# Kernel tuning notes

Hardware: AMD Instinct MI355X
Metric: run time of the kernel (lower is better)

## Reference

```python
import jax, jax.numpy as jnp
import numpy as np

DIM = 512
HEADS = 8
DIM_HEAD = 64
SCALE = DIM_HEAD ** -0.5


def setup_inputs() -> dict:
    key = jax.random.key(0)
    k1, k2, k3, k4, k5 = jax.random.split(key, 5)
    inner = HEADS * DIM_HEAD
    x = jax.random.normal(k1, (16, DIM, 32, 32), dtype=jnp.float32)
    W_proj = jax.random.normal(k2, (DIM, inner * 3), dtype=jnp.float32) * (DIM ** -0.5)
    b_proj = jax.random.normal(k3, (inner * 3,), dtype=jnp.float32) * 0.01
    W_out = jax.random.normal(k4, (inner, DIM), dtype=jnp.float32) * (inner ** -0.5)
    b_out = jax.random.normal(k5, (DIM,), dtype=jnp.float32) * 0.01
    return {"x": x, "W_proj": W_proj, "b_proj": b_proj, "W_out": W_out, "b_out": b_out}


def reference(x, W_proj, b_proj, W_out, b_out):
    b, c, hh, ww = x.shape
    s = hh * ww
    xs = x.reshape(b, c, s).transpose(0, 2, 1)  # b s c
    qkv = xs @ W_proj + b_proj                  # b s (heads * 3*dim_head)
    qkv = qkv.reshape(b, s, HEADS, 3 * DIM_HEAD)
    q, k, v = jnp.split(qkv, 3, axis=-1)        # each: b s h d
    w = jnp.einsum('bshd,bthd->bsth', q, k) * SCALE
    w = jax.nn.softmax(w, axis=2)
    res = jnp.einsum('bsth,bthd->bshd', w, v).reshape(b, s, HEADS * DIM_HEAD)
    out = res @ W_out + b_out + xs              # b s c (residual)
    return out.transpose(0, 2, 1).reshape(b, c, hh, ww)
```

## Files before the change

kernel.cpp:

```cpp
#include <hip/hip_runtime.h>
#include <hip/hip_bf16.h>

#define BATCH 16
#define CDIM  512
#define SEQ   1024
#define HEADS 8
#define DHEAD 64
#define N3    1536
#define QSCALE 0.18033688011112042f

typedef unsigned short ushort_t;
typedef __attribute__((ext_vector_type(8))) short short8;
typedef __attribute__((ext_vector_type(4))) float f32x4;

__device__ __forceinline__ unsigned f2bf(float f) {
    unsigned u = __float_as_uint(f);
    u += 0x7fffu + ((u >> 16) & 1u);
    return u >> 16;
}
__device__ __forceinline__ float fast_exp2(float x) {
    float r;
    asm("v_exp_f32 %0, %1" : "=v"(r) : "v"(x));
    return r;
}
__device__ __forceinline__ unsigned pack_bf16_trunc(float lo, float hi) {
    return __builtin_amdgcn_perm(__float_as_uint(hi), __float_as_uint(lo), 0x07060302u);
}
__device__ __forceinline__ void async16(const void* g, void* l) {
    __builtin_amdgcn_global_load_lds(
        (const __attribute__((address_space(1))) unsigned int*)g,
        (__attribute__((address_space(3))) unsigned int*)l, 16, 0, 0);
}


__global__ __launch_bounds__(256) void blockify_kernel(
    const float* __restrict__ in, ushort_t* __restrict__ out, int C)
{
    __shared__ float t[64][65];
    const int k0 = blockIdx.y * 64, c0 = blockIdx.x * 64;
    const float* inb = in + (size_t)blockIdx.z * 512 * C;
    const int tid = threadIdx.x;
#pragma unroll
    for (int i = 0; i < 16; ++i) {
        int idx = tid + i * 256;
        int r = idx >> 6, c = idx & 63;
        t[r][c] = inb[(size_t)(k0 + r) * C + c0 + c];
    }
    __syncthreads();
    const size_t mbase = (size_t)blockIdx.z * C + c0;
    const int ml = tid & 63;
#pragma unroll
    for (int i = 0; i < 2; ++i) {
        int oct = (tid >> 6) + i * 4;
        size_t m = mbase + ml;
        int mt = (int)(m >> 7), mr = (int)(m & 127);
        int m16 = mr >> 4, col = mr & 15;
        int k = k0 + oct * 8;
        int it = k >> 5, q = (k >> 3) & 3;
        uint4 pk;
        pk.x = f2bf(t[oct * 8 + 0][ml]) | (f2bf(t[oct * 8 + 1][ml]) << 16);
        pk.y = f2bf(t[oct * 8 + 2][ml]) | (f2bf(t[oct * 8 + 3][ml]) << 16);
        pk.z = f2bf(t[oct * 8 + 4][ml]) | (f2bf(t[oct * 8 + 5][ml]) << 16);
        pk.w = f2bf(t[oct * 8 + 6][ml]) | (f2bf(t[oct * 8 + 7][ml]) << 16);
        size_t off = ((size_t)(mt * 16 + it) * 8 + m16) * 512 + (q * 16 + col) * 8;
        *(uint4*)&out[off] = pk;
    }
}

__global__ __launch_bounds__(256) void qkv_gemm_kernel(
    const ushort_t* __restrict__ xtb, const ushort_t* __restrict__ WpTb,
    const float* __restrict__ bp,
    ushort_t* __restrict__ q_buf, ushort_t* __restrict__ kb,
    ushort_t* __restrict__ vb)
{
    __shared__ alignas(16) ushort_t Asub[2][8 * 512];
    __shared__ alignas(16) ushort_t Bsub[2][8 * 512];

    const int tid = threadIdx.x, w = tid >> 6, lane = tid & 63;
    const int quad = lane >> 4, col = lane & 15;
    const int wm = w >> 1, wn = w & 1;

    const int lin = blockIdx.x + 12 * blockIdx.y;
    const int xcd = lin & 7;
    const int rr  = lin >> 3;
    const int n0  = (rr % 12) * 128;
    const int m0  = ((rr / 12) * 8 + xcd) * 128;

    f32x4 acc[4][4];
#pragma unroll
    for (int i = 0; i < 4; ++i)
#pragma unroll
        for (int j = 0; j < 4; ++j) acc[i][j] = (f32x4){0.f, 0.f, 0.f, 0.f};

    const ushort_t* Ab = xtb  + (size_t)(m0 >> 7) * 65536 + (w * 2) * 512 + lane * 8;
    const ushort_t* Bb = WpTb + (size_t)(n0 >> 7) * 65536 + (w * 2) * 512 + lane * 8;

#define QKV_STAGE(buf, it)                                        \
    do {                                                          \
        async16(Ab + (it) * 4096,       &Asub[buf][(w * 2 + 0) * 512]); \
        async16(Ab + (it) * 4096 + 512, &Asub[buf][(w * 2 + 1) * 512]); \
        async16(Bb + (it) * 4096,       &Bsub[buf][(w * 2 + 0) * 512]); \
        async16(Bb + (it) * 4096 + 512, &Bsub[buf][(w * 2 + 1) * 512]); \
    } while (0)

    QKV_STAGE(0, 0);
    for (int it = 0; it < 16; ++it) {
        const int cur = it & 1;
        __syncthreads();
        if (it < 15) QKV_STAGE(cur ^ 1, it + 1);

        short8 af[4], bfr[4];
#pragma unroll
        for (int i = 0; i < 4; ++i) af[i]  = *(const short8*)&Asub[cur][(wm * 4 + i) * 512 + lane * 8];
#pragma unroll
        for (int j = 0; j < 4; ++j) bfr[j] = *(const short8*)&Bsub[cur][(wn * 4 + j) * 512 + lane * 8];
#pragma unroll
        for (int i = 0; i < 4; ++i)
#pragma unroll
            for (int j = 0; j < 4; ++j)
                acc[i][j] = __builtin_amdgcn_mfma_f32_16x16x32_bf16(af[i], bfr[j], acc[i][j], 0, 0, 0);
    }
#undef QKV_STAGE

    const int b = m0 >> 10, s0 = m0 & 1023;
    const size_t b8 = (size_t)b * HEADS;
#pragma unroll
    for (int j = 0; j < 4; ++j) {
        int nb = n0 + wn * 64 + j * 16;
        int h = nb / 192, rem = nb % 192;
        int type = rem >> 6, dbase = rem & 63;
        float bias = bp[nb + col];
        size_t bh = b8 + h;
        int d = dbase + col;
#pragma unroll
        for (int i = 0; i < 4; ++i) {
            int sb = s0 + wm * 64 + i * 16 + quad * 4;
            f32x4 v = acc[i][j];
            if (type == 2) {
                unsigned lo = f2bf(v[0] + bias) | (f2bf(v[1] + bias) << 16);
                unsigned hi = f2bf(v[2] + bias) | (f2bf(v[3] + bias) << 16);
                uint2 pk; pk.x = lo; pk.y = hi;
                int itv = sb >> 6, sub = (d >> 4) * 2 + ((sb >> 5) & 1);
                size_t off = ((bh * 16 + itv) * 8 + sub) * 512
                           + (((sb >> 3) & 3) * 16 + (d & 15)) * 8 + (sb & 7);
                *(uint2*)&vb[off] = pk;
            } else if (type == 1) {
#pragma unroll
                for (int r = 0; r < 4; ++r) {
                    int t = sb + r;
                    int itk = t >> 6, sub = ((t >> 4) & 3) * 2 + (d >> 5);
                    size_t off = ((bh * 16 + itk) * 8 + sub) * 512
                               + (((d >> 3) & 3) * 16 + (t & 15)) * 8 + (d & 7);
                    kb[off] = (ushort_t)f2bf(v[r] + bias);
                }
            } else {
#pragma unroll
                for (int r = 0; r < 4; ++r)
                    q_buf[(bh * SEQ + sb + r) * DHEAD + d] =
                        (ushort_t)f2bf((v[r] + bias) * QSCALE);
            }
        }
    }
}

__global__ __launch_bounds__(128) void attn_kernel(
    const ushort_t* __restrict__ q_buf, const ushort_t* __restrict__ kb,
    const ushort_t* __restrict__ vb, ushort_t* __restrict__ resb)
{
    __shared__ alignas(16) ushort_t Kf[2][8 * 512];
    __shared__ alignas(16) ushort_t Vf[2][8 * 512];
    __shared__ alignas(16) ushort_t Pf[2 * 1024];

    const int tid  = threadIdx.x;
    const int w    = tid >> 6;
    const int lane = tid & 63;
    const int quad = lane >> 4;
    const int col  = lane & 15;

    const int bhid = blockIdx.x;
    const int b = bhid >> 3, h = bhid & 7;
    const int q0 = blockIdx.y * 128;
    const size_t bh = (size_t)b * HEADS + h;

    const ushort_t* qp = q_buf + ((bh * SEQ) + q0 + w * 64 + col) * DHEAD + quad * 8;
    short8 qf0[4], qf1[4];
#pragma unroll
    for (int g = 0; g < 4; ++g) {
        qf0[g] = *(const short8*)(qp + g * 16 * DHEAD);
        qf1[g] = *(const short8*)(qp + g * 16 * DHEAD + 32);
    }

    short8 ones;
#pragma unroll
    for (int i = 0; i < 8; ++i) ones[i] = (short)0x3F80;

    f32x4 O[4][4];
#pragma unroll
    for (int g = 0; g < 4; ++g)
#pragma unroll
        for (int i = 0; i < 4; ++i) O[g][i] = (f32x4){0.f, 0.f, 0.f, 0.f};
    f32x4 L[4];
#pragma unroll
    for (int g = 0; g < 4; ++g) L[g] = (f32x4){0.f, 0.f, 0.f, 0.f};

    const ushort_t* kaB = kb + (size_t)bh * 65536 + (w * 4) * 512 + lane * 8;
    const ushort_t* vaB = vb + (size_t)bh * 65536 + (w * 4) * 512 + lane * 8;

    const int poff_base = col * 8 + (quad & 1) * 4;
    const int qh = quad >> 1;
    ushort_t* pg = &Pf[w * 1024];

#define ATTN_STAGE(buf)                                            \
    do {                                                           \
        async16(kaB,        &Kf[buf][(w * 4 + 0) * 512]);          \
        async16(kaB + 512,  &Kf[buf][(w * 4 + 1) * 512]);          \
        async16(kaB + 1024, &Kf[buf][(w * 4 + 2) * 512]);          \
        async16(kaB + 1536, &Kf[buf][(w * 4 + 3) * 512]);          \
        async16(vaB,        &Vf[buf][(w * 4 + 0) * 512]);          \
        async16(vaB + 512,  &Vf[buf][(w * 4 + 1) * 512]);          \
        async16(vaB + 1024, &Vf[buf][(w * 4 + 2) * 512]);          \
        async16(vaB + 1536, &Vf[buf][(w * 4 + 3) * 512]);          \
        kaB += 4096;                                               \
        vaB += 4096;                                               \
    } while (0)

    ATTN_STAGE(0);

    for (int it = 0; it < 16; ++it) {
        const int cur = it & 1;
        const ushort_t* kc = Kf[cur];
        const ushort_t* vc = Vf[cur];
        __syncthreads();
        if (it < 15) ATTN_STAGE(cur ^ 1);

        short8 kf[8];
#pragma unroll
        for (int t16 = 0; t16 < 4; ++t16) {
            kf[2 * t16 + 0] = *(const short8*)&kc[(t16 * 2 + 0) * 512 + lane * 8];
            kf[2 * t16 + 1] = *(const short8*)&kc[(t16 * 2 + 1) * 512 + lane * 8];
        }

        short8 pf[4][2];
#pragma unroll
        for (int g = 0; g < 4; ++g) {
            f32x4 S[4];
            __builtin_amdgcn_s_setprio(1);
#pragma unroll
            for (int t16 = 0; t16 < 4; ++t16) {
                f32x4 a = (f32x4){0.f, 0.f, 0.f, 0.f};
                a = __builtin_amdgcn_mfma_f32_16x16x32_bf16(kf[2 * t16 + 0], qf0[g], a, 0, 0, 0);
                a = __builtin_amdgcn_mfma_f32_16x16x32_bf16(kf[2 * t16 + 1], qf1[g], a, 0, 0, 0);
                S[t16] = a;
            }
            __builtin_amdgcn_s_setprio(0);
#pragma unroll
            for (int t16 = 0; t16 < 4; ++t16) {
                uint2 pk;
                pk.x = pack_bf16_trunc(fast_exp2(S[t16][0]), fast_exp2(S[t16][1]));
                pk.y = pack_bf16_trunc(fast_exp2(S[t16][2]), fast_exp2(S[t16][3]));
                int off = (t16 >> 1) * 512 + (((t16 * 2) + qh) & 3) * 128 + poff_base;
                *(uint2*)&pg[off] = pk;
            }
            pf[g][0] = *(const short8*)&pg[lane * 8];
            pf[g][1] = *(const short8*)&pg[512 + lane * 8];
        }

#pragma unroll
        for (int d16 = 0; d16 < 4; ++d16) {
            const short8 v0 = *(const short8*)&vc[(d16 * 2 + 0) * 512 + lane * 8];
            const short8 v1 = *(const short8*)&vc[(d16 * 2 + 1) * 512 + lane * 8];
            __builtin_amdgcn_s_setprio(1);
#pragma unroll
            for (int g = 0; g < 4; ++g) {
                O[g][d16] = __builtin_amdgcn_mfma_f32_16x16x32_bf16(pf[g][0], v0, O[g][d16], 0, 0, 0);
                O[g][d16] = __builtin_amdgcn_mfma_f32_16x16x32_bf16(pf[g][1], v1, O[g][d16], 0, 0, 0);
            }
            __builtin_amdgcn_s_setprio(0);
        }
#pragma unroll
        for (int g = 0; g < 4; ++g) {
            L[g] = __builtin_amdgcn_mfma_f32_16x16x32_bf16(pf[g][0], ones, L[g], 0, 0, 0);
            L[g] = __builtin_amdgcn_mfma_f32_16x16x32_bf16(pf[g][1], ones, L[g], 0, 0, 0);
        }
    }
#undef ATTN_STAGE

    const int mt = b * 8 + (q0 >> 7);
#pragma unroll
    for (int g = 0; g < 4; ++g) {
        const int m16 = w * 4 + g;
#pragma unroll
        for (int r = 0; r < 4; ++r) {
            float inv = 1.f / L[g][r];
            const int mcol = quad * 4 + r;
#pragma unroll
            for (int d16 = 0; d16 < 4; ++d16) {
                int itk = h * 2 + (d16 >> 1);
                int kq = (d16 & 1) * 2 + (col >> 3);
                size_t off = ((size_t)(mt * 16 + itk) * 8 + m16) * 512
                           + (kq * 16 + mcol) * 8 + (col & 7);
                resb[off] = (ushort_t)f2bf(O[g][d16][r] * inv);
            }
        }
    }
}

__global__ __launch_bounds__(256) void out_gemm_kernel(
    const ushort_t* __restrict__ resb, const ushort_t* __restrict__ WoTb,
    const float* __restrict__ bo, const float* __restrict__ x,
    float* __restrict__ out)
{
    __shared__ alignas(16) ushort_t Asub[2][8 * 512];
    __shared__ alignas(16) ushort_t Bsub[2][8 * 512];

    const int tid = threadIdx.x, w = tid >> 6, lane = tid & 63;
    const int quad = lane >> 4, col = lane & 15;
    const int wm = w >> 1, wn = w & 1;

    const int lin = blockIdx.x + 4 * blockIdx.y;
    const int xcd = lin & 7;
    const int rr  = lin >> 3;
    const int n0  = (rr & 3) * 128;
    const int m0  = ((rr >> 2) * 8 + xcd) * 128;

    f32x4 acc[4][4];
#pragma unroll
    for (int i = 0; i < 4; ++i)
#pragma unroll
        for (int j = 0; j < 4; ++j) acc[i][j] = (f32x4){0.f, 0.f, 0.f, 0.f};

    const ushort_t* Ab = resb + (size_t)(m0 >> 7) * 65536 + (w * 2) * 512 + lane * 8;
    const ushort_t* Bb = WoTb + (size_t)(n0 >> 7) * 65536 + (w * 2) * 512 + lane * 8;

#define OUT_STAGE(buf, it)                                        \
    do {                                                          \
        async16(Ab + (it) * 4096,       &Asub[buf][(w * 2 + 0) * 512]); \
        async16(Ab + (it) * 4096 + 512, &Asub[buf][(w * 2 + 1) * 512]); \
        async16(Bb + (it) * 4096,       &Bsub[buf][(w * 2 + 0) * 512]); \
        async16(Bb + (it) * 4096 + 512, &Bsub[buf][(w * 2 + 1) * 512]); \
    } while (0)

    OUT_STAGE(0, 0);
    for (int it = 0; it < 16; ++it) {
        const int cur = it & 1;
        __syncthreads();
        if (it < 15) OUT_STAGE(cur ^ 1, it + 1);

        short8 af[4], bfr[4];
#pragma unroll
        for (int i = 0; i < 4; ++i) af[i]  = *(const short8*)&Asub[cur][(wm * 4 + i) * 512 + lane * 8];
#pragma unroll
        for (int j = 0; j < 4; ++j) bfr[j] = *(const short8*)&Bsub[cur][(wn * 4 + j) * 512 + lane * 8];
#pragma unroll
        for (int i = 0; i < 4; ++i)
#pragma unroll
            for (int j = 0; j < 4; ++j)
                acc[i][j] = __builtin_amdgcn_mfma_f32_16x16x32_bf16(af[i], bfr[j], acc[i][j], 0, 0, 0);
    }
#undef OUT_STAGE

    const int b = m0 >> 10, s0 = m0 & 1023;
#pragma unroll
    for (int j = 0; j < 4; ++j) {
        int n = n0 + wn * 64 + j * 16 + col;
        float bias = bo[n];
#pragma unroll
        for (int i = 0; i < 4; ++i) {
            int sb = s0 + wm * 64 + i * 16 + quad * 4;
            size_t o = ((size_t)b * CDIM + n) * SEQ + sb;
            float4 xr = *(const float4*)&x[o];
            f32x4 v = acc[i][j];
            float4 ov;
            ov.x = v[0] + bias + xr.x;
            ov.y = v[1] + bias + xr.y;
            ov.z = v[2] + bias + xr.z;
            ov.w = v[3] + bias + xr.w;
            *(float4*)&out[o] = ov;
        }
    }
}

extern "C" void kernel_launch(void* const* d_in, const int* in_sizes, int n_in,
                              void* d_out, int out_size, void* d_ws, size_t ws_size,
                              hipStream_t stream) {
    const float* x  = (const float*)d_in[0];
    const float* Wp = (const float*)d_in[1];
    const float* bp = (const float*)d_in[2];
    const float* Wo = (const float*)d_in[3];
    const float* bo = (const float*)d_in[4];
    float* out = (float*)d_out;

    ushort_t* xtb   = (ushort_t*)d_ws;
    ushort_t* WpTb  = xtb   + (size_t)8388608;
    ushort_t* WoTb  = WpTb  + (size_t)786432;
    ushort_t* q_buf = WoTb  + (size_t)262144;
    ushort_t* kb    = q_buf + (size_t)8388608;
    ushort_t* vb    = kb    + (size_t)8388608;
    ushort_t* resb  = vb    + (size_t)8388608;

    blockify_kernel<<<dim3(16, 8, 16), 256, 0, stream>>>(x,  xtb,  1024);
    blockify_kernel<<<dim3(24, 8, 1),  256, 0, stream>>>(Wp, WpTb, 1536);
    blockify_kernel<<<dim3(8, 8, 1),   256, 0, stream>>>(Wo, WoTb, 512);
    qkv_gemm_kernel<<<dim3(12, 128), 256, 0, stream>>>(xtb, WpTb, bp, q_buf, kb, vb);
    attn_kernel<<<dim3(128, 8), 128, 0, stream>>>(q_buf, kb, vb, resb);
    out_gemm_kernel<<<dim3(4, 128), 256, 0, stream>>>(resb, WoTb, bo, x, out);
}
```

Baseline: 195.0 us.

## Prefetch two stages ahead with partial vmcnt waits instead of full syncthreads

In the QKV GEMM, attention and output GEMM loops, two async global-to-LDS stages are now kept in flight. Each iteration waits only for the older stage with a partial s_waitcnt vmcnt followed by a raw barrier, instead of a __syncthreads that drains all outstanding loads. A second barrier after compute protects the buffer before it is refilled two iterations ahead. This aims to hide more global load latency, at the cost of an extra barrier per iteration and reliance on the hand-written vmcnt counts matching the number of issued loads.

```diff
diff --git a/kernel.cpp b/kernel.cpp
--- a/kernel.cpp
+++ b/kernel.cpp
@@ -31,6 +31,12 @@
         (const __attribute__((address_space(1))) unsigned int*)g,
         (__attribute__((address_space(3))) unsigned int*)l, 16, 0, 0);
 }
+__device__ __forceinline__ void barrier_raw() {
+    __builtin_amdgcn_sched_barrier(0);
+    __builtin_amdgcn_s_barrier();
+    __builtin_amdgcn_sched_barrier(0);
+}
+#define WAIT_VMCNT(n) asm volatile("s_waitcnt vmcnt(" #n ")" ::: "memory")
 
 
 __global__ __launch_bounds__(256) void blockify_kernel(
@@ -95,19 +101,20 @@
     const ushort_t* Ab = xtb  + (size_t)(m0 >> 7) * 65536 + (w * 2) * 512 + lane * 8;
     const ushort_t* Bb = WpTb + (size_t)(n0 >> 7) * 65536 + (w * 2) * 512 + lane * 8;
 
-#define QKV_STAGE(buf, it)                                        \
+#define QKV_STAGE(buf, t)                                         \
     do {                                                          \
-        async16(Ab + (it) * 4096,       &Asub[buf][(w * 2 + 0) * 512]); \
-        async16(Ab + (it) * 4096 + 512, &Asub[buf][(w * 2 + 1) * 512]); \
-        async16(Bb + (it) * 4096,       &Bsub[buf][(w * 2 + 0) * 512]); \
-        async16(Bb + (it) * 4096 + 512, &Bsub[buf][(w * 2 + 1) * 512]); \
+        async16(Ab + (t) * 4096,       &Asub[buf][(w * 2 + 0) * 512]); \
+        async16(Ab + (t) * 4096 + 512, &Asub[buf][(w * 2 + 1) * 512]); \
+        async16(Bb + (t) * 4096,       &Bsub[buf][(w * 2 + 0) * 512]); \
+        async16(Bb + (t) * 4096 + 512, &Bsub[buf][(w * 2 + 1) * 512]); \
     } while (0)
 
     QKV_STAGE(0, 0);
+    QKV_STAGE(1, 1);
     for (int it = 0; it < 16; ++it) {
         const int cur = it & 1;
-        __syncthreads();
-        if (it < 15) QKV_STAGE(cur ^ 1, it + 1);
+        if (it < 15) { WAIT_VMCNT(4); } else { WAIT_VMCNT(0); }
+        barrier_raw();
 
         short8 af[4], bfr[4];
 #pragma unroll
@@ -119,6 +126,11 @@
 #pragma unroll
             for (int j = 0; j < 4; ++j)
                 acc[i][j] = __builtin_amdgcn_mfma_f32_16x16x32_bf16(af[i], bfr[j], acc[i][j], 0, 0, 0);
+
+        if (it < 14) {
+            barrier_raw();
+            QKV_STAGE(cur, it + 2);
+        }
     }
 #undef QKV_STAGE
 
@@ -210,28 +222,29 @@
     const int qh = quad >> 1;
     ushort_t* pg = &Pf[w * 1024];
 
-#define ATTN_STAGE(buf)                                            \
-    do {                                                           \
-        async16(kaB,        &Kf[buf][(w * 4 + 0) * 512]);          \
-        async16(kaB + 512,  &Kf[buf][(w * 4 + 1) * 512]);          \
-        async16(kaB + 1024, &Kf[buf][(w * 4 + 2) * 512]);          \
-        async16(kaB + 1536, &Kf[buf][(w * 4 + 3) * 512]);          \
-        async16(vaB,        &Vf[buf][(w * 4 + 0) * 512]);          \
-        async16(vaB + 512,  &Vf[buf][(w * 4 + 1) * 512]);          \
-        async16(vaB + 1024, &Vf[buf][(w * 4 + 2) * 512]);          \
-        async16(vaB + 1536, &Vf[buf][(w * 4 + 3) * 512]);          \
-        kaB += 4096;                                               \
-        vaB += 4096;                                               \
+#define ATTN_STAGE(buf, t)                                          \
+    do {                                                            \
+        const ushort_t* ka_ = kaB + (size_t)(t) * 4096;             \
+        const ushort_t* va_ = vaB + (size_t)(t) * 4096;             \
+        async16(ka_,        &Kf[buf][(w * 4 + 0) * 512]);           \
+        async16(ka_ + 512,  &Kf[buf][(w * 4 + 1) * 512]);           \
+        async16(ka_ + 1024, &Kf[buf][(w * 4 + 2) * 512]);           \
+        async16(ka_ + 1536, &Kf[buf][(w * 4 + 3) * 512]);           \
+        async16(va_,        &Vf[buf][(w * 4 + 0) * 512]);           \
+        async16(va_ + 512,  &Vf[buf][(w * 4 + 1) * 512]);           \
+        async16(va_ + 1024, &Vf[buf][(w * 4 + 2) * 512]);           \
+        async16(va_ + 1536, &Vf[buf][(w * 4 + 3) * 512]);           \
     } while (0)
 
-    ATTN_STAGE(0);
+    ATTN_STAGE(0, 0);
+    ATTN_STAGE(1, 1);
 
     for (int it = 0; it < 16; ++it) {
         const int cur = it & 1;
         const ushort_t* kc = Kf[cur];
         const ushort_t* vc = Vf[cur];
-        __syncthreads();
-        if (it < 15) ATTN_STAGE(cur ^ 1);
+        if (it < 15) { WAIT_VMCNT(8); } else { WAIT_VMCNT(0); }
+        barrier_raw();
 
         short8 kf[8];
 #pragma unroll
@@ -282,6 +295,11 @@
             L[g] = __builtin_amdgcn_mfma_f32_16x16x32_bf16(pf[g][0], ones, L[g], 0, 0, 0);
             L[g] = __builtin_amdgcn_mfma_f32_16x16x32_bf16(pf[g][1], ones, L[g], 0, 0, 0);
         }
+
+        if (it < 14) {
+            barrier_raw();
+            ATTN_STAGE(cur, it + 2);
+        }
     }
 #undef ATTN_STAGE
 
@@ -332,19 +350,20 @@
     const ushort_t* Ab = resb + (size_t)(m0 >> 7) * 65536 + (w * 2) * 512 + lane * 8;
     const ushort_t* Bb = WoTb + (size_t)(n0 >> 7) * 65536 + (w * 2) * 512 + lane * 8;
 
-#define OUT_STAGE(buf, it)                                        \
+#define OUT_STAGE(buf, t)                                         \
     do {                                                          \
-        async16(Ab + (it) * 4096,       &Asub[buf][(w * 2 + 0) * 512]); \
-        async16(Ab + (it) * 4096 + 512, &Asub[buf][(w * 2 + 1) * 512]); \
-        async16(Bb + (it) * 4096,       &Bsub[buf][(w * 2 + 0) * 512]); \
-        async16(Bb + (it) * 4096 + 512, &Bsub[buf][(w * 2 + 1) * 512]); \
+        async16(Ab + (t) * 4096,       &Asub[buf][(w * 2 + 0) * 512]); \
+        async16(Ab + (t) * 4096 + 512, &Asub[buf][(w * 2 + 1) * 512]); \
+        async16(Bb + (t) * 4096,       &Bsub[buf][(w * 2 + 0) * 512]); \
+        async16(Bb + (t) * 4096 + 512, &Bsub[buf][(w * 2 + 1) * 512]); \
     } while (0)
 
     OUT_STAGE(0, 0);
+    OUT_STAGE(1, 1);
     for (int it = 0; it < 16; ++it) {
         const int cur = it & 1;
-        __syncthreads();
-        if (it < 15) OUT_STAGE(cur ^ 1, it + 1);
+        if (it < 15) { WAIT_VMCNT(4); } else { WAIT_VMCNT(0); }
+        barrier_raw();
 
         short8 af[4], bfr[4];
 #pragma unroll
@@ -356,6 +375,11 @@
 #pragma unroll
             for (int j = 0; j < 4; ++j)
                 acc[i][j] = __builtin_amdgcn_mfma_f32_16x16x32_bf16(af[i], bfr[j], acc[i][j], 0, 0, 0);
+
+        if (it < 14) {
+            barrier_raw();
+            OUT_STAGE(cur, it + 2);
+        }
     }
 #undef OUT_STAGE
 
```

New measurement: 194.0 us. Within noise of the previous version (-0.6%).
